# Optimization experiments

Hardware: AMD Instinct MI355X
Metric: run time of the kernel (lower is better)

The kernel has to match this reference:

```python
import jax, jax.numpy as jnp
import numpy as np
from jax import lax

N, CIN, COUT, H, W = 16, 512, 256, 32, 32
EPS = 1e-5


def _conv(x, w, b, pad_h, pad_w):
    # x: [N,Cin,H,W], w: [Cout,Cin,kh,kw], pad = ((top,bottom),(left,right))
    y = lax.conv_general_dilated(
        x, w, window_strides=(1, 1), padding=(pad_h, pad_w),
        dimension_numbers=("NCHW", "OIHW", "NCHW"))
    return y + b[None, :, None, None]


def setup_inputs() -> dict:
    key = jax.random.key(0)
    ks = jax.random.split(key, 12)
    s = 0.02
    return {
        "x": jax.random.normal(ks[0], (N, CIN, H, W), jnp.float32),
        "w1": jax.random.normal(ks[1], (COUT, CIN, 3, 3), jnp.float32) * s,
        "b1": jax.random.normal(ks[2], (COUT,), jnp.float32) * s,
        "w2": jax.random.normal(ks[3], (COUT, CIN, 2, 3), jnp.float32) * s,
        "b2": jax.random.normal(ks[4], (COUT,), jnp.float32) * s,
        "w3": jax.random.normal(ks[5], (COUT, CIN, 3, 2), jnp.float32) * s,
        "b3": jax.random.normal(ks[6], (COUT,), jnp.float32) * s,
        "w4": jax.random.normal(ks[7], (COUT, CIN, 2, 2), jnp.float32) * s,
        "b4": jax.random.normal(ks[8], (COUT,), jnp.float32) * s,
        "gamma": jnp.ones((COUT,), jnp.float32),
        "beta": jnp.zeros((COUT,), jnp.float32),
    }


def reference(x, w1, b1, w2, b2, w3, b3, w4, b4, gamma, beta):
    # torch F.pad(l,r,t,b) -> lax padding ((top,bottom),(left,right))
    o1 = _conv(x, w1, b1, (1, 1), (1, 1))  # 3x3, pad (1,1,1,1) -> [N,Cout,H,W]
    o2 = _conv(x, w2, b2, (1, 0), (1, 1))  # 2x3, pad (1,1,1,0)
    o3 = _conv(x, w3, b3, (1, 1), (1, 0))  # 3x2, pad (1,0,1,1)
    o4 = _conv(x, w4, b4, (1, 0), (1, 0))  # 2x2, pad (1,0,1,0)
    # pixel-shuffle interleave: o1->(even,even), o2->(odd,even), o3->(even,odd), o4->(odd,odd)
    row_even = jnp.stack([o1, o3], axis=-1).reshape(N, COUT, H, 2 * W)
    row_odd = jnp.stack([o2, o4], axis=-1).reshape(N, COUT, H, 2 * W)
    y = jnp.stack([row_even, row_odd], axis=-2).reshape(N, COUT, 2 * H, 2 * W)
    # BatchNorm2d, training mode: biased batch stats over (N,H,W)
    mean = jnp.mean(y, axis=(0, 2, 3), keepdims=True)
    var = jnp.mean(jnp.square(y - mean), axis=(0, 2, 3), keepdims=True)
    normed = (y - mean) * lax.rsqrt(var + EPS)
    normed = normed * gamma[None, :, None, None] + beta[None, :, None, None]
    return jax.nn.relu(normed)
```

## Files before the change

### kernel.cpp

```cpp
#include <hip/hip_runtime.h>
#include <hip/hip_bf16.h>


typedef unsigned short ushort_t;
typedef __attribute__((ext_vector_type(8))) short short8;
typedef __attribute__((ext_vector_type(4))) float floatx4;
typedef __attribute__((ext_vector_type(2))) float floatx2;
typedef __attribute__((ext_vector_type(4))) unsigned short u16x4;
typedef __attribute__((ext_vector_type(8))) unsigned short u16x8;
typedef __attribute__((ext_vector_type(4))) unsigned int u32x4;

#define XT_OFF    0u
#define WT_OFF    18939904u
#define BIAS_OFF  28377088u
#define STATS_OFF 28381184u

#define NSITES_P0 204
#define NSITES_P1 170

#define ASYNC16(g, l) __builtin_amdgcn_global_load_lds( \
    (const __attribute__((address_space(1))) void*)(g), \
    (__attribute__((address_space(3))) void*)(l), 16, 0, 0)

#define ISSUE_FENCE asm volatile("" ::: "memory")

#define WAITBAR4 \
  asm volatile("s_waitcnt vmcnt(4) lgkmcnt(0)\n\ts_barrier" ::: "memory")
#define WAITBAR0 \
  asm volatile("s_waitcnt vmcnt(0) lgkmcnt(0)\n\ts_barrier" ::: "memory")

__device__ __forceinline__ ushort_t f2bf(float f) {
  unsigned int u = __builtin_bit_cast(unsigned int, f);
  u += 0x7fffu + ((u >> 16) & 1u);
  return (ushort_t)(u >> 16);
}

__global__ __launch_bounds__(256) void prep_all(
    const float* __restrict__ x, ushort_t* __restrict__ xt,
    const float* __restrict__ w1, const float* __restrict__ w2,
    const float* __restrict__ w3, const float* __restrict__ w4,
    const float* __restrict__ b1, const float* __restrict__ b2,
    const float* __restrict__ b3, const float* __restrict__ b4,
    ushort_t* __restrict__ wt, float* __restrict__ bias,
    float* __restrict__ stats) {
  __shared__ ushort_t lds[128 * 36];
  const int blk = blockIdx.x;
  const int t = threadIdx.x;
  if (blk < 1024) {
    const int q = blk >> 8, co = blk & 255;
    const int row = ((q & 1) << 9) + (co << 1) + (q >> 1);
    if (blk == 0) { stats[t] = 0.f; stats[t + 256] = 0.f; }
    const float* wsrc; const float* bsrc; int khl, kwl;
    if (q == 0)      { wsrc = w1; bsrc = b1; khl = 3; kwl = 3; }
    else if (q == 1) { wsrc = w2; bsrc = b2; khl = 2; kwl = 3; }
    else if (q == 2) { wsrc = w3; bsrc = b3; khl = 3; kwl = 2; }
    else             { wsrc = w4; bsrc = b4; khl = 2; kwl = 2; }
    if (t == 0) bias[row] = bsrc[co];
    ushort_t* dst = wt + (size_t)row * 4608;
    for (int tap = 0; tap < 9; ++tap) {
      const int dh = tap / 3, dw = tap % 3;
      const bool valid = (dh < khl) && (dw < kwl);
#pragma unroll
      for (int cc = 0; cc < 2; ++cc) {
        const int ci = cc * 256 + t;
        ushort_t v = 0;
        if (valid)
          v = f2bf(wsrc[(((size_t)co * 512 + ci) * khl + dh) * kwl + dw]);
        dst[tap * 512 + ci] = v;
      }
    }
    return;
  }
  const int idx = blk - 1024;
  const int n = idx / 136;
  const int rem = idx % 136;
  const int hp = rem >> 2;
  const int ci0 = (rem & 3) << 7;
  ushort_t* dst = xt + (size_t)(n * 34 + hp) * (34 * 512);
  if (hp == 0 || hp == 33) {
    u32x4 z = {0u, 0u, 0u, 0u};
    for (int i = t; i < 544; i += 256)
      ((u32x4*)(dst + (i >> 4) * 512 + ci0))[i & 15] = z;
    return;
  }
  const int h = hp - 1;
  if (t < 32) {
    u32x4 z = {0u, 0u, 0u, 0u};
    const int w = (t >> 4) ? 33 : 0;
    ((u32x4*)(dst + w * 512 + ci0))[t & 15] = z;
  }
  const size_t base = (size_t)n * 524288 + (size_t)h * 32;
  {
    const int cil = t >> 3;
    const int w4 = (t & 7) << 2;
#pragma unroll
    for (int cc = 0; cc < 4; ++cc) {
      const int ci = cil + cc * 32;
      floatx4 v = *(const floatx4*)(x + base + (size_t)(ci0 + ci) * 1024 + w4);
      u16x4 hv;
#pragma unroll
      for (int j = 0; j < 4; ++j) hv[j] = f2bf(v[j]);
      *(u16x4*)&lds[ci * 36 + w4] = hv;
    }
  }
  __syncthreads();
  {
    const int w = t & 31;
    const int j8 = t >> 5;
#pragma unroll
    for (int cc2 = 0; cc2 < 2; ++cc2) {
      const int cil2 = cc2 * 64 + j8 * 8;
      u16x8 v;
#pragma unroll
      for (int j = 0; j < 8; ++j) v[j] = lds[(cil2 + j) * 36 + w];
      *(u16x8*)(dst + (w + 1) * 512 + ci0 + cil2) = v;
    }
  }
}

template <int NTAPS, int NSITES_T>
__device__ __forceinline__ void gemm_body(
    const ushort_t* __restrict__ xt, const ushort_t* __restrict__ wt,
    const float* __restrict__ bias, float* __restrict__ out,
    float* __restrict__ stats, char* ldsX, char* ldsW,
    int bn, int bm) {
  const int tid = threadIdx.x;
  const int n0 = bn << 7;
  const int n_img = bm >> 3;
  const int h0p = (bm & 7) << 2;
  const int wv = tid >> 6, lane = tid & 63;
  const int ri = lane & 15, kg = lane >> 4;
  const int wm = (wv & 1) << 6, wn = (wv >> 1) << 6;

  constexpr int XTOT = NSITES_T * 8;
  constexpr int XFP = XTOT / 256;
  constexpr int XTL = XTOT - XFP * 256;

  const char* xgp[XFP + 1];
  char* xlp[XFP + 1];
  {
    const char* xg = (const char*)(xt + (size_t)(n_img * 34 + h0p) * (34 * 512));
#pragma unroll
    for (int p = 0; p < XFP + 1; ++p) {
      const int idx = p * 256 + tid;
      const int site = idx >> 3, slot = idx & 7;
      const int c = slot ^ (site & 7);
      xgp[p] = xg + site * 1024 + (c << 4);
      xlp[p] = ldsX + idx * 16;
    }
  }
  const char* wgp[4];
#pragma unroll
  for (int p = 0; p < 4; ++p) {
    const int idx = p * 256 + tid;
    const int row = idx >> 3, slot = idx & 7;
    const int c = slot ^ (row & 7);
    wgp[p] = (const char*)wt + (size_t)(n0 + row) * 9216 + (c << 4);
  }
  char* const wl = ldsW + tid * 16;

  floatx4 acc[4][4] = {};

  int arow[4], bsite[4];
#pragma unroll
  for (int f = 0; f < 4; ++f) arow[f] = wn + (f << 4) + ri;
#pragma unroll
  for (int fj = 0; fj < 4; ++fj)
    bsite[fj] = ((wm >> 5) + (fj >> 1)) * 34 + ((fj & 1) << 4) + ri;

  for (int chunk = 0; chunk < 8; ++chunk) {
    const int cb = chunk << 7;
#pragma unroll
    for (int p = 0; p < XFP; ++p) ASYNC16(xgp[p] + cb, xlp[p]);
    if (tid < XTL) ASYNC16(xgp[XFP] + cb, xlp[XFP]);
    ISSUE_FENCE;
#pragma unroll
    for (int p = 0; p < 4; ++p) ASYNC16(wgp[p] + cb, wl + p * 4096);
    ISSUE_FENCE;
#pragma unroll
    for (int p = 0; p < 4; ++p)
      ASYNC16(wgp[p] + cb + 1024, wl + 16384 + p * 4096);
    WAITBAR4;
#pragma unroll
    for (int tap = 0; tap < NTAPS; ++tap) {
      if (tap + 2 < NTAPS) {
        const int noff = ((tap + 2) << 10) + cb;
        char* const wld = ldsW + ((tap + 2) % 3) * 16384 + tid * 16;
#pragma unroll
        for (int p = 0; p < 4; ++p) ASYNC16(wgp[p] + noff, wld + p * 4096);
      }
      const char* wb = ldsW + (tap % 3) * 16384;
      const int tsite = (tap / 3) * 34 + (tap % 3);
#pragma unroll
      for (int ks = 0; ks < 2; ++ks) {
        const int c = (ks << 2) + kg;
        short8 a4[4], b4[4];
#pragma unroll
        for (int f = 0; f < 4; ++f)
          a4[f] = *(const short8*)(wb + arow[f] * 128 +
                                   ((c ^ (arow[f] & 7)) << 4));
#pragma unroll
        for (int fj = 0; fj < 4; ++fj) {
          const int srow = bsite[fj] + tsite;
          b4[fj] = *(const short8*)(ldsX + srow * 128 + ((c ^ (srow & 7)) << 4));
        }
#pragma unroll
        for (int fi = 0; fi < 4; ++fi)
#pragma unroll
          for (int fj = 0; fj < 4; ++fj)
            acc[fi][fj] = __builtin_amdgcn_mfma_f32_16x16x32_bf16(
                a4[fi], b4[fj], acc[fi][fj], 0, 0, 0);
      }
      if (tap + 2 < NTAPS) { WAITBAR4; } else { WAITBAR0; }
    }
  }

  const int quad = kg, colL = ri;
  const int dh6 = (bn >> 2) << 6;
#pragma unroll
  for (int fi = 0; fi < 4; ++fi) {
    const int rbase = n0 + wn + (fi << 4) + (quad << 2);
    const floatx4 bv = *(const floatx4*)(bias + rbase);
    const int co = (rbase & 511) >> 1;
    float sA = 0.f, s2A = 0.f, sB = 0.f, s2B = 0.f;
    float* ob = out + (((size_t)(n_img * 256 + co)) << 12) + dh6;
#pragma unroll
    for (int fj = 0; fj < 4; ++fj) {
      const int mb = wm + (fj << 4) + colL;
      const int h = h0p + (mb >> 5), w = mb & 31;
      const float v0 = acc[fi][fj][0] + bv[0];
      const float v1 = acc[fi][fj][1] + bv[1];
      const float v2 = acc[fi][fj][2] + bv[2];
      const float v3 = acc[fi][fj][3] + bv[3];
      sA += v0 + v1;
      s2A += v0 * v0 + v1 * v1;
      sB += v2 + v3;
      s2B += v2 * v2 + v3 * v3;
      float* p = ob + (h << 7) + (w << 1);
      floatx2 eA = {v0, v1};
      floatx2 eB = {v2, v3};
      *(floatx2*)p = eA;
      *(floatx2*)(p + 4096) = eB;
    }
#pragma unroll
    for (int off = 1; off < 16; off <<= 1) {
      sA += __shfl_xor(sA, off);
      s2A += __shfl_xor(s2A, off);
      sB += __shfl_xor(sB, off);
      s2B += __shfl_xor(s2B, off);
    }
    if (colL == 0) {
      atomicAdd(&stats[co], sA);
      atomicAdd(&stats[256 + co], s2A);
      atomicAdd(&stats[co + 1], sB);
      atomicAdd(&stats[256 + co + 1], s2B);
    }
  }
}

__global__ __launch_bounds__(256) void gemm_kernel(
    const ushort_t* __restrict__ xt, const ushort_t* __restrict__ wt,
    const float* __restrict__ bias, float* __restrict__ out,
    float* __restrict__ stats) {
  __shared__ char ldsX[NSITES_P0 * 128];
  __shared__ char ldsW[3][128 * 128];
  const int bx = blockIdx.x;
  const int bn = (bx & 7) ^ (((bx >> 9) & 1) << 2);
  const int bm = (bx >> 3) & 127;
  if (bn < 4)
    gemm_body<9, NSITES_P0>(xt, wt, bias, out, stats,
                            ldsX, ldsW[0], bn, bm);
  else
    gemm_body<6, NSITES_P1>(xt, wt, bias, out, stats,
                            ldsX, ldsW[0], bn, bm);
}

__global__ __launch_bounds__(256) void bn_apply(
    float* __restrict__ y, const float* __restrict__ stats,
    const float* __restrict__ gamma, const float* __restrict__ beta) {
  const int b = blockIdx.x;
  const int co = b & 255;
  const int t = threadIdx.x;
  const float mean = stats[co] * (1.f / 65536.f);
  const float var = stats[256 + co] * (1.f / 65536.f) - mean * mean;
  const float rstd = rsqrtf(var + 1e-5f);
  const float scale = rstd * gamma[co];
  const float shift = beta[co] - mean * scale;
  float* p = y + (size_t)b * 4096;
#pragma unroll
  for (int it = 0; it < 4; ++it) {
    floatx4* q = (floatx4*)(p + (it * 256 + t) * 4);
    floatx4 v = *q;
#pragma unroll
    for (int e = 0; e < 4; ++e) v[e] = fmaxf(v[e] * scale + shift, 0.f);
    *q = v;
  }
}

extern "C" void kernel_launch(void* const* d_in, const int* in_sizes, int n_in,
                              void* d_out, int out_size, void* d_ws,
                              size_t ws_size, hipStream_t stream) {
  const float* x  = (const float*)d_in[0];
  const float* w1 = (const float*)d_in[1];
  const float* b1 = (const float*)d_in[2];
  const float* w2 = (const float*)d_in[3];
  const float* b2 = (const float*)d_in[4];
  const float* w3 = (const float*)d_in[5];
  const float* b3 = (const float*)d_in[6];
  const float* w4 = (const float*)d_in[7];
  const float* b4 = (const float*)d_in[8];
  const float* gamma = (const float*)d_in[9];
  const float* beta  = (const float*)d_in[10];
  float* out = (float*)d_out;

  char* ws = (char*)d_ws;
  ushort_t* xt   = (ushort_t*)(ws + XT_OFF);
  ushort_t* wt   = (ushort_t*)(ws + WT_OFF);
  float*    bias = (float*)(ws + BIAS_OFF);
  float*    st   = (float*)(ws + STATS_OFF);

  prep_all<<<3200, 256, 0, stream>>>(x, xt, w1, w2, w3, w4,
                                     b1, b2, b3, b4, wt, bias, st);
  gemm_kernel<<<1024, 256, 0, stream>>>(xt, wt, bias, out, st);
  bn_apply<<<4096, 256, 0, stream>>>(out, st, gamma, beta);
}
```

Before: 261.6 us.

## Load weight fragments directly from global memory instead of staging through LDS

Removes the triple-buffered LDS staging of weight tiles and the asynchronous prefetch pipeline. Each wave now loads its weight MFMA fragments straight from global memory (relying on caches) and only the input tile goes through LDS, with plain __syncthreads per chunk. This shrinks LDS use from about 74KB to about 26KB so more blocks can be resident (launch bounds now ask for 3 per SIMD). The trade is uncoalesced, latency-exposed global loads in the inner tap loop and the loss of load/compute overlap for weights.

```diff
diff --git a/kernel.cpp b/kernel.cpp
--- a/kernel.cpp
+++ b/kernel.cpp
@@ -21,13 +21,6 @@
 #define ASYNC16(g, l) __builtin_amdgcn_global_load_lds( \
     (const __attribute__((address_space(1))) void*)(g), \
     (__attribute__((address_space(3))) void*)(l), 16, 0, 0)
-
-#define ISSUE_FENCE asm volatile("" ::: "memory")
-
-#define WAITBAR4 \
-  asm volatile("s_waitcnt vmcnt(4) lgkmcnt(0)\n\ts_barrier" ::: "memory")
-#define WAITBAR0 \
-  asm volatile("s_waitcnt vmcnt(0) lgkmcnt(0)\n\ts_barrier" ::: "memory")
 
 __device__ __forceinline__ ushort_t f2bf(float f) {
   unsigned int u = __builtin_bit_cast(unsigned int, f);
@@ -122,8 +115,7 @@
 __device__ __forceinline__ void gemm_body(
     const ushort_t* __restrict__ xt, const ushort_t* __restrict__ wt,
     const float* __restrict__ bias, float* __restrict__ out,
-    float* __restrict__ stats, char* ldsX, char* ldsW,
-    int bn, int bm) {
+    float* __restrict__ stats, char* ldsX, int bn, int bm) {
   const int tid = threadIdx.x;
   const int n0 = bn << 7;
   const int n_img = bm >> 3;
@@ -149,56 +141,41 @@
       xlp[p] = ldsX + idx * 16;
     }
   }
-  const char* wgp[4];
-#pragma unroll
-  for (int p = 0; p < 4; ++p) {
-    const int idx = p * 256 + tid;
-    const int row = idx >> 3, slot = idx & 7;
-    const int c = slot ^ (row & 7);
-    wgp[p] = (const char*)wt + (size_t)(n0 + row) * 9216 + (c << 4);
-  }
-  char* const wl = ldsW + tid * 16;
+  const char* wbase = (const char*)wt;
+  unsigned int wrow[4];
+#pragma unroll
+  for (int f = 0; f < 4; ++f)
+    wrow[f] = (unsigned int)(n0 + wn + (f << 4) + ri) * 9216u;
 
   floatx4 acc[4][4] = {};
 
-  int arow[4], bsite[4];
-#pragma unroll
-  for (int f = 0; f < 4; ++f) arow[f] = wn + (f << 4) + ri;
+  int bsite[4];
 #pragma unroll
   for (int fj = 0; fj < 4; ++fj)
     bsite[fj] = ((wm >> 5) + (fj >> 1)) * 34 + ((fj & 1) << 4) + ri;
 
   for (int chunk = 0; chunk < 8; ++chunk) {
     const int cb = chunk << 7;
+    __syncthreads();
 #pragma unroll
     for (int p = 0; p < XFP; ++p) ASYNC16(xgp[p] + cb, xlp[p]);
     if (tid < XTL) ASYNC16(xgp[XFP] + cb, xlp[XFP]);
-    ISSUE_FENCE;
-#pragma unroll
-    for (int p = 0; p < 4; ++p) ASYNC16(wgp[p] + cb, wl + p * 4096);
-    ISSUE_FENCE;
-#pragma unroll
-    for (int p = 0; p < 4; ++p)
-      ASYNC16(wgp[p] + cb + 1024, wl + 16384 + p * 4096);
-    WAITBAR4;
+    __syncthreads();
 #pragma unroll
     for (int tap = 0; tap < NTAPS; ++tap) {
-      if (tap + 2 < NTAPS) {
-        const int noff = ((tap + 2) << 10) + cb;
-        char* const wld = ldsW + ((tap + 2) % 3) * 16384 + tid * 16;
-#pragma unroll
-        for (int p = 0; p < 4; ++p) ASYNC16(wgp[p] + noff, wld + p * 4096);
-      }
-      const char* wb = ldsW + (tap % 3) * 16384;
+      const unsigned int toff = (unsigned int)(tap << 10) + cb;
       const int tsite = (tap / 3) * 34 + (tap % 3);
+      short8 aw[2][4];
+#pragma unroll
+      for (int ks = 0; ks < 2; ++ks)
+#pragma unroll
+        for (int f = 0; f < 4; ++f)
+          aw[ks][f] = *(const short8*)(
+              wbase + wrow[f] + toff + (((ks << 2) + kg) << 4));
 #pragma unroll
       for (int ks = 0; ks < 2; ++ks) {
         const int c = (ks << 2) + kg;
-        short8 a4[4], b4[4];
-#pragma unroll
-        for (int f = 0; f < 4; ++f)
-          a4[f] = *(const short8*)(wb + arow[f] * 128 +
-                                   ((c ^ (arow[f] & 7)) << 4));
+        short8 b4[4];
 #pragma unroll
         for (int fj = 0; fj < 4; ++fj) {
           const int srow = bsite[fj] + tsite;
@@ -209,9 +186,8 @@
 #pragma unroll
           for (int fj = 0; fj < 4; ++fj)
             acc[fi][fj] = __builtin_amdgcn_mfma_f32_16x16x32_bf16(
-                a4[fi], b4[fj], acc[fi][fj], 0, 0, 0);
+                aw[ks][fi], b4[fj], acc[fi][fj], 0, 0, 0);
       }
-      if (tap + 2 < NTAPS) { WAITBAR4; } else { WAITBAR0; }
     }
   }
 
@@ -258,21 +234,18 @@
   }
 }
 
-__global__ __launch_bounds__(256) void gemm_kernel(
+__global__ __launch_bounds__(256, 3) void gemm_kernel(
     const ushort_t* __restrict__ xt, const ushort_t* __restrict__ wt,
     const float* __restrict__ bias, float* __restrict__ out,
     float* __restrict__ stats) {
   __shared__ char ldsX[NSITES_P0 * 128];
-  __shared__ char ldsW[3][128 * 128];
   const int bx = blockIdx.x;
   const int bn = (bx & 7) ^ (((bx >> 9) & 1) << 2);
   const int bm = (bx >> 3) & 127;
   if (bn < 4)
-    gemm_body<9, NSITES_P0>(xt, wt, bias, out, stats,
-                            ldsX, ldsW[0], bn, bm);
+    gemm_body<9, NSITES_P0>(xt, wt, bias, out, stats, ldsX, bn, bm);
   else
-    gemm_body<6, NSITES_P1>(xt, wt, bias, out, stats,
-                            ldsX, ldsW[0], bn, bm);
+    gemm_body<6, NSITES_P1>(xt, wt, bias, out, stats, ldsX, bn, bm);
 }
 
 __global__ __launch_bounds__(256) void bn_apply(
```

After: 499.7 us. +91.0%, slower.

## Halve K-chunk to 64 channels to shrink LDS and raise occupancy

Applied to the files above, without the earlier changes.

Each implicit-GEMM chunk now covers 64 input channels instead of 128. That halves the LDS footprint for the X tile and the triple-buffered weight taps, and the new launch bound asks for 4 blocks per CU. The swizzled LDS layout is reworked so two sites or rows share one 128-byte line, and the global-to-LDS address mapping and wait counts are updated to match. In exchange there are twice as many chunk iterations, barriers and X-tile reloads, with fewer MFMAs between each sync, and the launch bound may force register spills.

```diff
diff --git a/kernel.cpp b/kernel.cpp
--- a/kernel.cpp
+++ b/kernel.cpp
@@ -24,8 +24,8 @@
 
 #define ISSUE_FENCE asm volatile("" ::: "memory")
 
-#define WAITBAR4 \
-  asm volatile("s_waitcnt vmcnt(4) lgkmcnt(0)\n\ts_barrier" ::: "memory")
+#define WAITBAR2 \
+  asm volatile("s_waitcnt vmcnt(2) lgkmcnt(0)\n\ts_barrier" ::: "memory")
 #define WAITBAR0 \
   asm volatile("s_waitcnt vmcnt(0) lgkmcnt(0)\n\ts_barrier" ::: "memory")
 
@@ -132,7 +132,7 @@
   const int ri = lane & 15, kg = lane >> 4;
   const int wm = (wv & 1) << 6, wn = (wv >> 1) << 6;
 
-  constexpr int XTOT = NSITES_T * 8;
+  constexpr int XTOT = NSITES_T * 4;
   constexpr int XFP = XTOT / 256;
   constexpr int XTL = XTOT - XFP * 256;
 
@@ -143,75 +143,79 @@
 #pragma unroll
     for (int p = 0; p < XFP + 1; ++p) {
       const int idx = p * 256 + tid;
-      const int site = idx >> 3, slot = idx & 7;
-      const int c = slot ^ (site & 7);
-      xgp[p] = xg + site * 1024 + (c << 4);
+      const int ss = idx >> 3, slot = idx & 7;
+      const int c8 = slot ^ (ss & 7);
+      xgp[p] = xg + ss * 2048 + ((c8 >> 2) << 10) + ((c8 & 3) << 4);
       xlp[p] = ldsX + idx * 16;
     }
   }
-  const char* wgp[4];
-#pragma unroll
-  for (int p = 0; p < 4; ++p) {
+  const char* wgp[2];
+#pragma unroll
+  for (int p = 0; p < 2; ++p) {
     const int idx = p * 256 + tid;
-    const int row = idx >> 3, slot = idx & 7;
-    const int c = slot ^ (row & 7);
-    wgp[p] = (const char*)wt + (size_t)(n0 + row) * 9216 + (c << 4);
+    const int ss = idx >> 3, slot = idx & 7;
+    const int c8 = slot ^ (ss & 7);
+    wgp[p] = (const char*)wt + (size_t)(n0 + 2 * ss + (c8 >> 2)) * 9216 +
+             ((c8 & 3) << 4);
   }
   char* const wl = ldsW + tid * 16;
 
   floatx4 acc[4][4] = {};
 
-  int arow[4], bsite[4];
-#pragma unroll
-  for (int f = 0; f < 4; ++f) arow[f] = wn + (f << 4) + ri;
+  int aoff[4];
+#pragma unroll
+  for (int f = 0; f < 4; ++f) {
+    const int r = wn + (f << 4) + ri;
+    const int ssa = r >> 1;
+    const int c8 = ((r & 1) << 2) | kg;
+    aoff[f] = ssa * 128 + ((c8 ^ (ssa & 7)) << 4);
+  }
+  int bsite[4];
 #pragma unroll
   for (int fj = 0; fj < 4; ++fj)
     bsite[fj] = ((wm >> 5) + (fj >> 1)) * 34 + ((fj & 1) << 4) + ri;
 
-  for (int chunk = 0; chunk < 8; ++chunk) {
-    const int cb = chunk << 7;
+  for (int chunk = 0; chunk < 16; ++chunk) {
+    const int cb = chunk << 6;
 #pragma unroll
     for (int p = 0; p < XFP; ++p) ASYNC16(xgp[p] + cb, xlp[p]);
     if (tid < XTL) ASYNC16(xgp[XFP] + cb, xlp[XFP]);
     ISSUE_FENCE;
 #pragma unroll
-    for (int p = 0; p < 4; ++p) ASYNC16(wgp[p] + cb, wl + p * 4096);
+    for (int p = 0; p < 2; ++p) ASYNC16(wgp[p] + cb, wl + p * 4096);
     ISSUE_FENCE;
 #pragma unroll
-    for (int p = 0; p < 4; ++p)
-      ASYNC16(wgp[p] + cb + 1024, wl + 16384 + p * 4096);
-    WAITBAR4;
+    for (int p = 0; p < 2; ++p)
+      ASYNC16(wgp[p] + cb + 1024, wl + 8192 + p * 4096);
+    WAITBAR2;
 #pragma unroll
     for (int tap = 0; tap < NTAPS; ++tap) {
       if (tap + 2 < NTAPS) {
         const int noff = ((tap + 2) << 10) + cb;
-        char* const wld = ldsW + ((tap + 2) % 3) * 16384 + tid * 16;
-#pragma unroll
-        for (int p = 0; p < 4; ++p) ASYNC16(wgp[p] + noff, wld + p * 4096);
+        char* const wld = ldsW + ((tap + 2) % 3) * 8192 + tid * 16;
+#pragma unroll
+        for (int p = 0; p < 2; ++p) ASYNC16(wgp[p] + noff, wld + p * 4096);
       }
-      const char* wb = ldsW + (tap % 3) * 16384;
+      const char* wb = ldsW + (tap % 3) * 8192;
       const int tsite = (tap / 3) * 34 + (tap % 3);
-#pragma unroll
-      for (int ks = 0; ks < 2; ++ks) {
-        const int c = (ks << 2) + kg;
-        short8 a4[4], b4[4];
-#pragma unroll
-        for (int f = 0; f < 4; ++f)
-          a4[f] = *(const short8*)(wb + arow[f] * 128 +
-                                   ((c ^ (arow[f] & 7)) << 4));
-#pragma unroll
-        for (int fj = 0; fj < 4; ++fj) {
-          const int srow = bsite[fj] + tsite;
-          b4[fj] = *(const short8*)(ldsX + srow * 128 + ((c ^ (srow & 7)) << 4));
-        }
-#pragma unroll
-        for (int fi = 0; fi < 4; ++fi)
-#pragma unroll
-          for (int fj = 0; fj < 4; ++fj)
-            acc[fi][fj] = __builtin_amdgcn_mfma_f32_16x16x32_bf16(
-                a4[fi], b4[fj], acc[fi][fj], 0, 0, 0);
+      short8 a4[4], b4[4];
+#pragma unroll
+      for (int f = 0; f < 4; ++f)
+        a4[f] = *(const short8*)(wb + aoff[f]);
+#pragma unroll
+      for (int fj = 0; fj < 4; ++fj) {
+        const int srow = bsite[fj] + tsite;
+        const int ssb = srow >> 1;
+        const int c8 = ((srow & 1) << 2) | kg;
+        b4[fj] = *(const short8*)(ldsX + ssb * 128 + ((c8 ^ (ssb & 7)) << 4));
       }
-      if (tap + 2 < NTAPS) { WAITBAR4; } else { WAITBAR0; }
+#pragma unroll
+      for (int fi = 0; fi < 4; ++fi)
+#pragma unroll
+        for (int fj = 0; fj < 4; ++fj)
+          acc[fi][fj] = __builtin_amdgcn_mfma_f32_16x16x32_bf16(
+              a4[fi], b4[fj], acc[fi][fj], 0, 0, 0);
+      if (tap + 2 < NTAPS) { WAITBAR2; } else { WAITBAR0; }
     }
   }
 
@@ -258,12 +262,12 @@
   }
 }
 
-__global__ __launch_bounds__(256) void gemm_kernel(
+__global__ __launch_bounds__(256, 4) void gemm_kernel(
     const ushort_t* __restrict__ xt, const ushort_t* __restrict__ wt,
     const float* __restrict__ bias, float* __restrict__ out,
     float* __restrict__ stats) {
-  __shared__ char ldsX[NSITES_P0 * 128];
-  __shared__ char ldsW[3][128 * 128];
+  __shared__ char ldsX[NSITES_P0 * 64];
+  __shared__ char ldsW[3][128 * 64];
   const int bx = blockIdx.x;
   const int bn = (bx & 7) ^ (((bx >> 9) & 1) << 2);
   const int bm = (bx >> 3) & 127;
```

New measurement: 280.4 us. 7.2% more time.
